# Kernel optimization log

Hardware: AMD Instinct MI355X
Metric: run time of the kernel (lower is better)

The kernel has to match this reference:

```python
import jax, jax.numpy as jnp
import numpy as np

B, FEW, NN = 4096, 5, 64
D = 128            # embed_dim
NSYM = 100000
DM = 2 * D         # d_model = 256
DI = 2 * DM        # support-encoder inner = 512
H = 2 * DM         # LSTMCell hidden = 512
STEPS = 4          # process_steps


def setup_inputs() -> dict:
    key = jax.random.key(0)
    cnt = [0]
    def nk():
        cnt[0] += 1
        return jax.random.fold_in(key, cnt[0])
    def nrm(shape, scale=0.05):
        return jax.random.normal(nk(), shape, dtype=jnp.float32) * scale
    def ridx(shape):
        return jax.random.randint(nk(), shape, 0, NSYM, dtype=jnp.int32)
    inp = {}
    inp['q_l1'] = ridx((B, NN, 2)); inp['q_l2'] = ridx((B, NN, 2))
    inp['q_r1'] = ridx((B, NN, 2)); inp['q_r2'] = ridx((B, NN, 2))
    inp['s_l1'] = ridx((FEW, NN, 2)); inp['s_l2'] = ridx((FEW, NN, 2))
    inp['s_r1'] = ridx((FEW, NN, 2)); inp['s_r2'] = ridx((FEW, NN, 2))
    inp['q_deg_l'] = jax.random.randint(nk(), (B,), 1, NN, dtype=jnp.int32)
    inp['q_deg_r'] = jax.random.randint(nk(), (B,), 1, NN, dtype=jnp.int32)
    inp['s_deg_l'] = jax.random.randint(nk(), (FEW,), 1, NN, dtype=jnp.int32)
    inp['s_deg_r'] = jax.random.randint(nk(), (FEW,), 1, NN, dtype=jnp.int32)
    inp['emb'] = nrm((NSYM + 1, D)).at[NSYM].set(0.0)  # padding_idx row = 0
    inp['gcn_w'] = nrm((D, 2 * D))
    inp['gcn_wb'] = nrm((D,))
    inp['gcn_b'] = jnp.zeros((D,), jnp.float32)
    inp['hop_gate'] = jnp.ones((2,), jnp.float32)
    inp['attn_w'] = nrm((1, D))
    inp['attn_b'] = jnp.zeros((1,), jnp.float32)
    inp['p1_w'] = nrm((DI, DM)); inp['p1_b'] = jnp.zeros((DI,), jnp.float32)
    inp['p2_w'] = nrm((DM, DI)); inp['p2_b'] = jnp.zeros((DM,), jnp.float32)
    inp['ln_g'] = jnp.ones((DM,), jnp.float32); inp['ln_b'] = jnp.zeros((DM,), jnp.float32)
    inp['w_ih'] = nrm((4 * H, DM)); inp['w_hh'] = nrm((4 * H, H))
    inp['b_ih'] = jnp.zeros((4 * H,), jnp.float32); inp['b_hh'] = jnp.zeros((4 * H,), jnp.float32)
    return inp


def _neighbor_encoder(conn, emb, gcn_w, gcn_wb, gcn_b, attn_w, attn_b):
    # conn: [N, NN, 2] (relation id, entity id)
    e = emb[conn]                                     # [N, NN, 2, D]
    concat = e.reshape(conn.shape[0], conn.shape[1], 2 * D)  # cat(rel, ent)
    proj = concat @ gcn_w.T + gcn_wb + gcn_b          # [N, NN, D]
    scores = (proj @ attn_w.T + attn_b)[..., 0]       # [N, NN]
    w = jax.nn.softmax(scores, axis=1)[..., None]
    return jnp.tanh(jnp.sum(proj * w, axis=1))        # [N, D]


def _support_encoder(x, p1_w, p1_b, p2_w, p2_b, ln_g, ln_b):
    out = jax.nn.relu(x @ p1_w.T + p1_b) @ p2_w.T + p2_b
    z = out + x
    mu = jnp.mean(z, axis=-1, keepdims=True)
    var = jnp.var(z, axis=-1, keepdims=True)
    return (z - mu) / jnp.sqrt(var + 1e-6) * ln_g + ln_b


def _query_encoder(support_g, q, w_ih, w_hh, b_ih, b_hh):
    # matching-networks 'process' LSTM attention, STEPS fixed iterations
    h_r = jnp.zeros((q.shape[0], H), q.dtype)
    c = jnp.zeros_like(h_r)
    h = q
    for _ in range(STEPS):
        gates = q @ w_ih.T + b_ih + h_r @ w_hh.T + b_hh
        i, f, g, o = jnp.split(gates, 4, axis=-1)
        c = jax.nn.sigmoid(f) * c + jax.nn.sigmoid(i) * jnp.tanh(g)
        h_cell = jax.nn.sigmoid(o) * jnp.tanh(c)
        h = q + h_cell[:, :DM]
        attn = jax.nn.softmax(h @ support_g.T, axis=1)
        r = attn @ support_g
        h_r = jnp.concatenate([h, r], axis=1)
    return h


def reference(q_l1, q_l2, q_r1, q_r2, s_l1, s_l2, s_r1, s_r2,
              q_deg_l, q_deg_r, s_deg_l, s_deg_r,
              emb, gcn_w, gcn_wb, gcn_b, hop_gate, attn_w, attn_b,
              p1_w, p1_b, p2_w, p2_b, ln_g, ln_b, w_ih, w_hh, b_ih, b_hh):
    ne = lambda conn: _neighbor_encoder(conn, emb, gcn_w, gcn_wb, gcn_b, attn_w, attn_b)
    gw = jax.nn.softmax(hop_gate)
    q_left = gw[0] * ne(q_l1) + gw[1] * ne(q_l2)
    q_right = gw[0] * ne(q_r1) + gw[1] * ne(q_r2)
    s_left = gw[0] * ne(s_l1) + gw[1] * ne(s_l2)
    s_right = gw[0] * ne(s_r1) + gw[1] * ne(s_r2)
    query_neighbor = jnp.concatenate([q_left, q_right], axis=-1)    # [B, DM]
    support_neighbor = jnp.concatenate([s_left, s_right], axis=-1)  # [FEW, DM]
    support_g = _support_encoder(support_neighbor, p1_w, p1_b, p2_w, p2_b, ln_g, ln_b)
    query_g = _query_encoder(support_g, query_neighbor, w_ih, w_hh, b_ih, b_hh)
    support_m = jnp.mean(support_g, axis=0, keepdims=True)          # [1, DM]
    return (query_g @ support_m.T)[:, 0]                            # [B]
```

## Files before the change

### kernel.cpp

```cpp
#include <hip/hip_runtime.h>

typedef unsigned short bf16u;
typedef unsigned char u8;
typedef unsigned int u32;
typedef float f32x4 __attribute__((ext_vector_type(4)));
typedef short bf16x8 __attribute__((ext_vector_type(8)));

__device__ inline float sigmoidf_(float x) { return 1.f / (1.f + __expf(-x)); }
__device__ inline float b2f(bf16u u) { return __uint_as_float(((u32)u) << 16); }
__device__ inline bf16u f2b(float f) {
  u32 i = __float_as_uint(f);
  u32 r = (i + 0x7fffu + ((i >> 16) & 1u)) >> 16;
  return (bf16u)r;
}
__device__ inline u8 enc8(float v) {
  float q = fmaf(v, 512.f, 128.5f);
  q = fminf(fmaxf(q, 0.f), 255.f);
  return (u8)(int)q;
}
__device__ inline float ub0(u32 u) { return (float)(u & 0xffu); }
__device__ inline float ub1(u32 u) { return (float)((u >> 8) & 0xffu); }
__device__ inline float ub2(u32 u) { return (float)((u >> 16) & 0xffu); }
__device__ inline float ub3(u32 u) { return (float)(u >> 24); }

__global__ __launch_bounds__(256) void k_prep(
    const float* __restrict__ gcn_w, const float* __restrict__ attn_w,
    const float* __restrict__ w_ih, const float* __restrict__ w_hh,
    const float* __restrict__ b_ih, const float* __restrict__ b_hh,
    bf16u* __restrict__ Vp, float* __restrict__ uvec,
    bf16u* __restrict__ WWa, bf16u* __restrict__ WWb, float* __restrict__ bsum,
    bf16u* __restrict__ XX)
{
  const int b = blockIdx.x, t = threadIdx.x;
  if (t < 59) XX[(size_t)b * 576 + 517 + t] = 0;
  if (b < 2048) {
    float wi = w_ih[b * 256 + t];
    float wh = w_hh[b * 512 + t];
    WWa[(size_t)b * 576 + t] = f2b(wi);
    WWb[(size_t)b * 576 + t] = f2b(wi + wh);
    WWb[(size_t)b * 576 + 256 + t] = f2b(wh);
    if (t < 59) WWb[(size_t)b * 576 + 517 + t] = 0;
    if (t == 0) bsum[b] = b_ih[b] + b_hh[b];
  } else if (b < 2304) {
    const int o = b - 2048;
    if (t < 128) Vp[o * 128 + t] = f2b(gcn_w[(o & 127) * 256 + ((o >> 7) << 7) + t]);
  } else if (b == 2304) {
    const int col = ((t >> 7) << 7) + (t & 127);
    float acc = 0.f;
    for (int d = 0; d < 128; ++d) acc += gcn_w[d * 256 + col] * attn_w[d];
    uvec[t] = acc;
  }
}

__global__ __launch_bounds__(256) void k_pre_gemm(
    const float* __restrict__ emb, const bf16u* __restrict__ Vp,
    const float* __restrict__ uvec,
    u8* __restrict__ pr, u8* __restrict__ pe,
    float* __restrict__ srel, float* __restrict__ sent)
{
  const int t = threadIdx.x;
  const int row0 = blockIdx.x << 6;
  __shared__ short As[64][136];
  __shared__ union PB {
    short B[128][136];
    u8 ob[64][272];
  } pb;
  __shared__ float us[256];
  us[t] = uvec[t];
  {
    const uint4* src = (const uint4*)Vp;
    #pragma unroll
    for (int s = 0; s < 8; ++s) {
      int f = s * 256 + t;
      *(uint4*)&pb.B[f >> 4][(f & 15) * 8] = src[f];
    }
  }
  #pragma unroll
  for (int s = 0; s < 8; ++s) {
    int f = s * 256 + t;
    int row = f >> 5, q = f & 31;
    int gr = row0 + row; if (gr > 100000) gr = 100000;
    float4 v = *(const float4*)&emb[(size_t)gr * 128 + (q << 2)];
    ushort4 pk;
    pk.x = f2b(v.x); pk.y = f2b(v.y); pk.z = f2b(v.z); pk.w = f2b(v.w);
    *(ushort4*)&As[row][q << 2] = pk;
  }
  __syncthreads();
  {
    const int row = t >> 2, l = t & 3;
    int gr = row0 + row; if (gr > 100000) gr = 100000;
    const short* ar = &As[row][l * 32];
    const float* u0 = &us[l * 32];
    const float* u1 = &us[128 + l * 32];
    float p0 = 0.f, p1 = 0.f;
    #pragma unroll
    for (int i = 0; i < 32; ++i) {
      float e = __uint_as_float(((u32)(unsigned short)ar[i]) << 16);
      p0 += e * u0[i];
      p1 += e * u1[i];
    }
    p0 += __shfl_xor(p0, 1, 64); p0 += __shfl_xor(p0, 2, 64);
    p1 += __shfl_xor(p1, 1, 64); p1 += __shfl_xor(p1, 2, 64);
    if (l == 0) { srel[gr] = p0; sent[gr] = p1; }
  }
  const int wave = t >> 6, lane = t & 63;
  const int quad = lane >> 4, l16 = lane & 15;
  const int wm = (wave >> 1) << 5, wn = (wave & 1) << 6;
  f32x4 acc0[2][4], acc1[2][4];
  #pragma unroll
  for (int i = 0; i < 2; ++i)
    #pragma unroll
    for (int j = 0; j < 4; ++j) {
      acc0[i][j] = (f32x4){0.f, 0.f, 0.f, 0.f};
      acc1[i][j] = (f32x4){0.f, 0.f, 0.f, 0.f};
    }
  #pragma unroll
  for (int kc = 0; kc < 4; ++kc) {
    bf16x8 af[2], bfr[4];
    #pragma unroll
    for (int i = 0; i < 2; ++i)
      af[i] = *(const bf16x8*)&As[wm + i * 16 + l16][kc * 32 + quad * 8];
    #pragma unroll
    for (int j = 0; j < 4; ++j)
      bfr[j] = *(const bf16x8*)&pb.B[wn + j * 16 + l16][kc * 32 + quad * 8];
    #pragma unroll
    for (int i = 0; i < 2; ++i)
      #pragma unroll
      for (int j = 0; j < 4; ++j)
        acc0[i][j] = __builtin_amdgcn_mfma_f32_16x16x32_bf16(af[i], bfr[j], acc0[i][j], 0, 0, 0);
  }
  __syncthreads();
  {
    const uint4* src = (const uint4*)(Vp + 128 * 128);
    #pragma unroll
    for (int s = 0; s < 8; ++s) {
      int f = s * 256 + t;
      *(uint4*)&pb.B[f >> 4][(f & 15) * 8] = src[f];
    }
  }
  __syncthreads();
  #pragma unroll
  for (int kc = 0; kc < 4; ++kc) {
    bf16x8 af[2], bfr[4];
    #pragma unroll
    for (int i = 0; i < 2; ++i)
      af[i] = *(const bf16x8*)&As[wm + i * 16 + l16][kc * 32 + quad * 8];
    #pragma unroll
    for (int j = 0; j < 4; ++j)
      bfr[j] = *(const bf16x8*)&pb.B[wn + j * 16 + l16][kc * 32 + quad * 8];
    #pragma unroll
    for (int i = 0; i < 2; ++i)
      #pragma unroll
      for (int j = 0; j < 4; ++j)
        acc1[i][j] = __builtin_amdgcn_mfma_f32_16x16x32_bf16(af[i], bfr[j], acc1[i][j], 0, 0, 0);
  }
  __syncthreads();
  #pragma unroll
  for (int j = 0; j < 4; ++j) {
    const int col = wn + j * 16 + l16;
    #pragma unroll
    for (int i = 0; i < 2; ++i) {
      #pragma unroll
      for (int r = 0; r < 4; ++r) {
        int row = wm + i * 16 + quad * 4 + r;
        pb.ob[row][col] = enc8(acc0[i][j][r]);
        pb.ob[row][128 + col] = enc8(acc1[i][j][r]);
      }
    }
  }
  __syncthreads();
  #pragma unroll
  for (int s = 0; s < 4; ++s) {
    int c = s * 256 + t;
    int row = c >> 4, part = c & 15;
    int gr = row0 + row;
    if (gr <= 100000) {
      uint4 v = *(const uint4*)&pb.ob[row][part * 16];
      if (part < 8) *(uint4*)&pr[(size_t)gr * 128 + part * 16] = v;
      else          *(uint4*)&pe[(size_t)gr * 128 + (part - 8) * 16] = v;
    }
  }
}

__global__ __launch_bounds__(256) void k_neighbor(
    const int* __restrict__ q_l1, const int* __restrict__ q_l2,
    const int* __restrict__ q_r1, const int* __restrict__ q_r2,
    const int* __restrict__ s_l1, const int* __restrict__ s_l2,
    const int* __restrict__ s_r1, const int* __restrict__ s_r2,
    const u8* __restrict__ pr, const u8* __restrict__ pe,
    const float* __restrict__ srel, const float* __restrict__ sent,
    const float* __restrict__ gcn_wb, const float* __restrict__ gcn_b,
    const float* __restrict__ hop_gate,
    float* __restrict__ qn, float* __restrict__ sn, bf16u* __restrict__ XX)
{
  const int b = blockIdx.x, t = threadIdx.x;
  const int *cA, *cB; float* outp; bf16u* xxp; int n, coloff;
  if (b < 4096)      { cA = q_l1; cB = q_l2; n = b;        outp = qn; xxp = XX; coloff = 0; }
  else if (b < 8192) { cA = q_r1; cB = q_r2; n = b - 4096; outp = qn; xxp = XX; coloff = 128; }
  else if (b < 8197) { cA = s_l1; cB = s_l2; n = b - 8192; outp = sn; xxp = 0;  coloff = 0; }
  else               { cA = s_r1; cB = s_r2; n = b - 8197; outp = sn; xxp = 0;  coloff = 128; }
  __shared__ int idxA[64][2], idxB[64][2];
  __shared__ float wA[64], wB[64];
  __shared__ float red[2][8][16][8];
  if (t < 128) {
    const int hop = t >> 6, nn = t & 63;
    const int* conn = hop ? cB : cA;
    int rel = conn[(n * 64 + nn) * 2 + 0];
    int ent = conn[(n * 64 + nn) * 2 + 1];
    int (*idx)[2] = hop ? idxB : idxA;
    idx[nn][0] = rel; idx[nn][1] = ent;
    float sc = srel[rel] + sent[ent];
    float m = sc;
    #pragma unroll
    for (int off = 32; off; off >>= 1) m = fmaxf(m, __shfl_xor(m, off, 64));
    float e = __expf(sc - m);
    float s = e;
    #pragma unroll
    for (int off = 32; off; off >>= 1) s += __shfl_xor(s, off, 64);
    (hop ? wB : wA)[nn] = e / s;
  }
  __syncthreads();
  {
    const int hop = t >> 7, g = (t >> 4) & 7, p = t & 15;
    const int (*idx)[2] = hop ? idxB : idxA;
    const float* w = hop ? wB : wA;
    uint2 ra[8], rb[8];
    #pragma unroll
    for (int kk = 0; kk < 8; ++kk) {
      int k = g + (kk << 3);
      ra[kk] = *(const uint2*)&pr[(size_t)idx[k][0] * 128 + p * 8];
      rb[kk] = *(const uint2*)&pe[(size_t)idx[k][1] * 128 + p * 8];
    }
    float a[8];
    #pragma unroll
    for (int c = 0; c < 8; ++c) a[c] = 0.f;
    #pragma unroll
    for (int kk = 0; kk < 8; ++kk) {
      float wk = w[g + (kk << 3)];
      a[0] += wk * (ub0(ra[kk].x) + ub0(rb[kk].x));
      a[1] += wk * (ub1(ra[kk].x) + ub1(rb[kk].x));
      a[2] += wk * (ub2(ra[kk].x) + ub2(rb[kk].x));
      a[3] += wk * (ub3(ra[kk].x) + ub3(rb[kk].x));
      a[4] += wk * (ub0(ra[kk].y) + ub0(rb[kk].y));
      a[5] += wk * (ub1(ra[kk].y) + ub1(rb[kk].y));
      a[6] += wk * (ub2(ra[kk].y) + ub2(rb[kk].y));
      a[7] += wk * (ub3(ra[kk].y) + ub3(rb[kk].y));
    }
    *(float4*)&red[hop][g][p][0] = (float4){a[0], a[1], a[2], a[3]};
    *(float4*)&red[hop][g][p][4] = (float4){a[4], a[5], a[6], a[7]};
  }
  __syncthreads();
  if (t < 128) {
    const int d = t, p = d >> 3, cq = d & 7;
    float sA = 0.f, sB = 0.f;
    #pragma unroll
    for (int g = 0; g < 8; ++g) {
      sA += red[0][g][p][cq];
      sB += red[1][g][p][cq];
    }
    float accA = sA * (1.f / 512.f) - 0.5f;
    float accB = sB * (1.f / 512.f) - 0.5f;
    float bias = gcn_wb[d] + gcn_b[d];
    float g0 = hop_gate[0], g1 = hop_gate[1];
    float mx = fmaxf(g0, g1);
    float e0 = __expf(g0 - mx), e1 = __expf(g1 - mx);
    float inv = 1.f / (e0 + e1);
    float v = e0 * inv * tanhf(bias + accA) + e1 * inv * tanhf(bias + accB);
    outp[n * 256 + coloff + d] = v;
    if (xxp) xxp[(size_t)n * 576 + coloff + d] = f2b(v);
  }
}

__global__ __launch_bounds__(256) void k_sup1(
    const float* __restrict__ sn, const float* __restrict__ p1_w,
    const float* __restrict__ p1_b, float* __restrict__ h1)
{
  const int r = blockIdx.x >> 3, j0 = (blockIdx.x & 7) << 6;
  const int t = threadIdx.x;
  __shared__ float xs[256];
  xs[t] = sn[r * 256 + t];
  __syncthreads();
  const int j = j0 + (t >> 2), q = t & 3;
  const float* wr = p1_w + (size_t)j * 256 + q * 64;
  float acc = 0.f;
  #pragma unroll
  for (int k = 0; k < 64; ++k) acc += xs[q * 64 + k] * wr[k];
  acc += __shfl_xor(acc, 1, 64);
  acc += __shfl_xor(acc, 2, 64);
  if (q == 0) h1[r * 512 + j] = fmaxf(acc + p1_b[j], 0.f);
}

__global__ __launch_bounds__(256) void k_sup2(
    const float* __restrict__ sn, const float* __restrict__ h1,
    const float* __restrict__ p2_w, const float* __restrict__ p2_b,
    const float* __restrict__ ln_g, const float* __restrict__ ln_b,
    float* __restrict__ sg)
{
  const int r = blockIdx.x, t = threadIdx.x;
  const int lane = t & 63, wave = t >> 6;
  __shared__ float hs[512];
  __shared__ float zs[256];
  __shared__ float r1[4], r2[4];
  hs[t] = h1[r * 512 + t];
  hs[t + 256] = h1[r * 512 + 256 + t];
  __syncthreads();
  const int q = t & 3;
  #pragma unroll
  for (int jc = 0; jc < 4; ++jc) {
    int j = jc * 64 + (t >> 2);
    const float* wr = p2_w + (size_t)j * 512 + q * 128;
    float acc = 0.f;
    #pragma unroll
    for (int k = 0; k < 128; ++k) acc += hs[q * 128 + k] * wr[k];
    acc += __shfl_xor(acc, 1, 64);
    acc += __shfl_xor(acc, 2, 64);
    if (q == 0) zs[j] = acc + p2_b[j] + sn[r * 256 + j];
  }
  __syncthreads();
  float v = zs[t];
  float s1 = v, s2 = v * v;
  #pragma unroll
  for (int off = 32; off; off >>= 1) { s1 += __shfl_xor(s1, off, 64); s2 += __shfl_xor(s2, off, 64); }
  if (lane == 0) { r1[wave] = s1; r2[wave] = s2; }
  __syncthreads();
  float S1 = r1[0] + r1[1] + r1[2] + r1[3];
  float S2 = r2[0] + r2[1] + r2[2] + r2[3];
  float mu = S1 * (1.f / 256.f);
  float var = S2 * (1.f / 256.f) - mu * mu;
  sg[r * 256 + t] = (v - mu) * rsqrtf(var + 1e-6f) * ln_g[t] + ln_b[t];
}

__global__ __launch_bounds__(256) void k_sg2(
    const float* __restrict__ sg, const float* __restrict__ w_hh,
    bf16u* __restrict__ WWb, float* __restrict__ sm)
{
  __shared__ float s[5][256];
  const int t = threadIdx.x;
  for (int i = t; i < 1280; i += 256) s[i >> 8][i & 255] = sg[i];
  __syncthreads();
  if (blockIdx.x == 0)
    sm[t] = (s[0][t] + s[1][t] + s[2][t] + s[3][t] + s[4][t]) * 0.2f;
  const int j = (blockIdx.x << 6) + (t >> 2), q = t & 3;
  const float4* wr = (const float4*)(w_hh + (size_t)j * 512 + 256 + q * 64);
  float a[5] = {0.f, 0.f, 0.f, 0.f, 0.f};
  #pragma unroll
  for (int kk = 0; kk < 16; ++kk) {
    float4 w = wr[kk];
    int k = q * 64 + kk * 4;
    #pragma unroll
    for (int r = 0; r < 5; ++r)
      a[r] += s[r][k] * w.x + s[r][k+1] * w.y + s[r][k+2] * w.z + s[r][k+3] * w.w;
  }
  #pragma unroll
  for (int r = 0; r < 5; ++r) {
    a[r] += __shfl_xor(a[r], 1, 64);
    a[r] += __shfl_xor(a[r], 2, 64);
  }
  if (q == 0) {
    #pragma unroll
    for (int r = 0; r < 5; ++r)
      WWb[(size_t)j * 576 + 512 + r] = f2b(a[r]);
  }
}

__global__ __launch_bounds__(256) void k_gates_mfma(
    const bf16u* __restrict__ XX, const bf16u* __restrict__ WW,
    const float* __restrict__ bsum, bf16u* __restrict__ gates, int kchunks)
{
  const int t = threadIdx.x;
  const int wave = t >> 6, lane = t & 63;
  const int quad = lane >> 4, l16 = lane & 15;
  const int wm = (wave >> 1) << 6, wn = (wave & 1) << 6;
  const int lin = (blockIdx.x & 7) * 64 + (blockIdx.x >> 3);
  const int row0 = (lin >> 4) << 7;
  const int col0 = (lin & 15) << 7;
  __shared__ short As[128][40];
  __shared__ short Bs[128][40];
  f32x4 acc[4][4];
  #pragma unroll
  for (int i = 0; i < 4; ++i)
    #pragma unroll
    for (int j = 0; j < 4; ++j) acc[i][j] = (f32x4){0.f, 0.f, 0.f, 0.f};

  const int srow = t >> 1, shalf = t & 1;
  const bf16u* xp = XX + (size_t)(row0 + srow) * 576 + shalf * 16;
  const bf16u* wp = WW + (size_t)(col0 + srow) * 576 + shalf * 16;

  uint4 x0 = *(const uint4*)(xp);
  uint4 x1 = *(const uint4*)(xp + 8);
  uint4 w0 = *(const uint4*)(wp);
  uint4 w1 = *(const uint4*)(wp + 8);

  for (int kc = 0; kc < kchunks; ++kc) {
    __syncthreads();
    *(uint4*)&As[srow][shalf * 16] = x0;
    *(uint4*)&As[srow][shalf * 16 + 8] = x1;
    *(uint4*)&Bs[srow][shalf * 16] = w0;
    *(uint4*)&Bs[srow][shalf * 16 + 8] = w1;
    __syncthreads();
    if (kc + 1 < kchunks) {
      x0 = *(const uint4*)(xp + (kc+1) * 32);
      x1 = *(const uint4*)(xp + (kc+1) * 32 + 8);
      w0 = *(const uint4*)(wp + (kc+1) * 32);
      w1 = *(const uint4*)(wp + (kc+1) * 32 + 8);
    }
    bf16x8 af[4], bfr[4];
    #pragma unroll
    for (int i = 0; i < 4; ++i)
      af[i] = *(const bf16x8*)&As[wm + i * 16 + l16][quad * 8];
    #pragma unroll
    for (int j = 0; j < 4; ++j)
      bfr[j] = *(const bf16x8*)&Bs[wn + j * 16 + l16][quad * 8];
    #pragma unroll
    for (int i = 0; i < 4; ++i)
      #pragma unroll
      for (int j = 0; j < 4; ++j)
        acc[i][j] = __builtin_amdgcn_mfma_f32_16x16x32_bf16(af[i], bfr[j], acc[i][j], 0, 0, 0);
  }

  #pragma unroll
  for (int j = 0; j < 4; ++j) {
    const int col = col0 + wn + j * 16 + l16;
    const float bs = bsum[col];
    #pragma unroll
    for (int i = 0; i < 4; ++i) {
      #pragma unroll
      for (int r = 0; r < 4; ++r) {
        int row = row0 + wm + i * 16 + quad * 4 + r;
        gates[(size_t)row * 2048 + col] = f2b(acc[i][j][r] + bs);
      }
    }
  }
}

__global__ __launch_bounds__(256) void k_cell(
    const bf16u* __restrict__ gates, const float* __restrict__ qn,
    float* __restrict__ c, bf16u* __restrict__ XX,
    const float* __restrict__ sg, const float* __restrict__ sm,
    float* __restrict__ out, int step)
{
  __shared__ float red[4][6];
  const int b = blockIdx.x, t = threadIdx.x;
  const int lane = t & 63, wave = t >> 6;
  const bf16u* g = gates + (size_t)b * 2048;
  float i0 = b2f(g[t]),       f0 = b2f(g[512 + t]), gg0 = b2f(g[1024 + t]), o0 = b2f(g[1536 + t]);
  float i1 = b2f(g[256 + t]), f1 = b2f(g[768 + t]), gg1 = b2f(g[1280 + t]);
  float co0 = step ? c[b * 512 + t] : 0.f;
  float co1 = step ? c[b * 512 + 256 + t] : 0.f;
  float c0 = sigmoidf_(f0) * co0 + sigmoidf_(i0) * tanhf(gg0);
  float c1 = sigmoidf_(f1) * co1 + sigmoidf_(i1) * tanhf(gg1);
  c[b * 512 + t] = c0;
  c[b * 512 + 256 + t] = c1;
  float hcv = sigmoidf_(o0) * tanhf(c0);
  float h = qn[b * 256 + t] + hcv;
  if (step < 3) {
    XX[(size_t)b * 576 + 256 + t] = f2b(hcv);
    float dots[5];
    #pragma unroll
    for (int s = 0; s < 5; ++s) dots[s] = h * sg[s * 256 + t];
    #pragma unroll
    for (int off = 32; off; off >>= 1) {
      #pragma unroll
      for (int s = 0; s < 5; ++s) dots[s] += __shfl_xor(dots[s], off, 64);
    }
    if (lane == 0) {
      #pragma unroll
      for (int s = 0; s < 5; ++s) red[wave][s] = dots[s];
    }
    __syncthreads();
    #pragma unroll
    for (int s = 0; s < 5; ++s)
      dots[s] = red[0][s] + red[1][s] + red[2][s] + red[3][s];
    float m = dots[0];
    #pragma unroll
    for (int s = 1; s < 5; ++s) m = fmaxf(m, dots[s]);
    float sum = 0.f;
    #pragma unroll
    for (int s = 0; s < 5; ++s) sum += __expf(dots[s] - m);
    if (t < 5) {
      float dv = (t == 1) ? dots[1] : (t == 2) ? dots[2] : (t == 3) ? dots[3]
               : (t == 4) ? dots[4] : dots[0];
      XX[(size_t)b * 576 + 512 + t] = f2b(__expf(dv - m) / sum);
    }
  } else {
    float v = h * sm[t];
    #pragma unroll
    for (int off = 32; off; off >>= 1) v += __shfl_xor(v, off, 64);
    if (lane == 0) red[wave][0] = v;
    __syncthreads();
    if (t == 0) out[b] = red[0][0] + red[1][0] + red[2][0] + red[3][0];
  }
}

extern "C" void kernel_launch(void* const* d_in, const int* in_sizes, int n_in,
                              void* d_out, int out_size, void* d_ws, size_t ws_size,
                              hipStream_t stream)
{
  (void)in_sizes; (void)n_in; (void)out_size; (void)ws_size;
  const int *q_l1 = (const int*)d_in[0], *q_l2 = (const int*)d_in[1];
  const int *q_r1 = (const int*)d_in[2], *q_r2 = (const int*)d_in[3];
  const int *s_l1 = (const int*)d_in[4], *s_l2 = (const int*)d_in[5];
  const int *s_r1 = (const int*)d_in[6], *s_r2 = (const int*)d_in[7];
  const float* emb      = (const float*)d_in[12];
  const float* gcn_w    = (const float*)d_in[13];
  const float* gcn_wb   = (const float*)d_in[14];
  const float* gcn_b    = (const float*)d_in[15];
  const float* hop_gate = (const float*)d_in[16];
  const float* attn_w   = (const float*)d_in[17];
  const float* p1_w = (const float*)d_in[19];
  const float* p1_b = (const float*)d_in[20];
  const float* p2_w = (const float*)d_in[21];
  const float* p2_b = (const float*)d_in[22];
  const float* ln_g = (const float*)d_in[23];
  const float* ln_b = (const float*)d_in[24];
  const float* w_ih = (const float*)d_in[25];
  const float* w_hh = (const float*)d_in[26];
  const float* b_ih = (const float*)d_in[27];
  const float* b_hh = (const float*)d_in[28];

  char* base = (char*)d_ws;
  size_t off = 0;
  auto alloc = [&](size_t bytes) -> char* {
    char* r = base + off;
    off = (off + bytes + 255) & ~(size_t)255;
    return r;
  };
  u8* pr       = (u8*)alloc(100001ull * 128);
  u8* pe       = (u8*)alloc(100001ull * 128);
  float* srel  = (float*)alloc(100001ull * 4);
  float* sent  = (float*)alloc(100001ull * 4);
  float* uvec  = (float*)alloc(256 * 4);
  bf16u* Vp    = (bf16u*)alloc(256 * 128 * 2);
  float* qn    = (float*)alloc(4096ull * 256 * 4);
  float* sn    = (float*)alloc(5 * 256 * 4);
  float* sg    = (float*)alloc(5 * 256 * 4);
  float* sm    = (float*)alloc(256 * 4);
  float* h1b   = (float*)alloc(5 * 512 * 4);
  bf16u* XX    = (bf16u*)alloc(4096ull * 576 * 2);
  bf16u* WWa   = (bf16u*)alloc(2048ull * 576 * 2);
  bf16u* WWb   = (bf16u*)alloc(2048ull * 576 * 2);
  float* bsum  = (float*)alloc(2048 * 4);
  bf16u* gates = (bf16u*)alloc(4096ull * 2048 * 2);
  float* cbuf  = (float*)alloc(4096ull * 512 * 4);

  k_prep<<<4096, 256, 0, stream>>>(gcn_w, attn_w, w_ih, w_hh, b_ih, b_hh,
                                   Vp, uvec, WWa, WWb, bsum, XX);
  k_pre_gemm<<<1563, 256, 0, stream>>>(emb, Vp, uvec, pr, pe, srel, sent);
  k_neighbor<<<8202, 256, 0, stream>>>(q_l1, q_l2, q_r1, q_r2, s_l1, s_l2, s_r1, s_r2,
                                       pr, pe, srel, sent, gcn_wb, gcn_b, hop_gate,
                                       qn, sn, XX);
  k_sup1<<<40, 256, 0, stream>>>(sn, p1_w, p1_b, h1b);
  k_sup2<<<5, 256, 0, stream>>>(sn, h1b, p2_w, p2_b, ln_g, ln_b, sg);
  k_sg2<<<32, 256, 0, stream>>>(sg, w_hh, WWb, sm);

  for (int step = 0; step < 4; ++step) {
    if (step == 0)
      k_gates_mfma<<<512, 256, 0, stream>>>(XX, WWa, bsum, gates, 8);
    else
      k_gates_mfma<<<512, 256, 0, stream>>>(XX, WWb, bsum, gates, 17);
    k_cell<<<4096, 256, 0, stream>>>(gates, qn, cbuf, XX, sg, sm, (float*)d_out, step);
  }
}
```

Before: 338.6 us.

## Precompute loop-invariant query gate contribution once and shrink per-step GEMM K

The query-neighbor part of the LSTM input, multiplied by (W_ih+W_hh) plus bias, is the same at every step. It is now computed once into a G1 buffer alongside the step-0 gates GEMM. Steps 1-3 then run a GEMM over K=320 (hidden state plus attention weights) and add G1 back, where before each step ran K=544 over the concatenated XX. This removes redundant MFMA work and operand reads per step, at the cost of a 16 MB bf16 G1 buffer read in each step's epilogue and an extra rounding to bf16.

```diff
diff --git a/kernel.cpp b/kernel.cpp
--- a/kernel.cpp
+++ b/kernel.cpp
@@ -28,18 +28,18 @@
     const float* __restrict__ w_ih, const float* __restrict__ w_hh,
     const float* __restrict__ b_ih, const float* __restrict__ b_hh,
     bf16u* __restrict__ Vp, float* __restrict__ uvec,
-    bf16u* __restrict__ WWa, bf16u* __restrict__ WWb, float* __restrict__ bsum,
-    bf16u* __restrict__ XX)
+    bf16u* __restrict__ WWa, bf16u* __restrict__ WWc, bf16u* __restrict__ WW2,
+    float* __restrict__ bsum, bf16u* __restrict__ XX2)
 {
   const int b = blockIdx.x, t = threadIdx.x;
-  if (t < 59) XX[(size_t)b * 576 + 517 + t] = 0;
+  if (t < 59) XX2[(size_t)b * 320 + 261 + t] = 0;
   if (b < 2048) {
     float wi = w_ih[b * 256 + t];
     float wh = w_hh[b * 512 + t];
-    WWa[(size_t)b * 576 + t] = f2b(wi);
-    WWb[(size_t)b * 576 + t] = f2b(wi + wh);
-    WWb[(size_t)b * 576 + 256 + t] = f2b(wh);
-    if (t < 59) WWb[(size_t)b * 576 + 517 + t] = 0;
+    WWa[(size_t)b * 256 + t] = f2b(wi);
+    WWc[(size_t)b * 256 + t] = f2b(wi + wh);
+    WW2[(size_t)b * 320 + t] = f2b(wh);
+    if (t < 59) WW2[(size_t)b * 320 + 261 + t] = 0;
     if (t == 0) bsum[b] = b_ih[b] + b_hh[b];
   } else if (b < 2304) {
     const int o = b - 2048;
@@ -267,7 +267,7 @@
     float inv = 1.f / (e0 + e1);
     float v = e0 * inv * tanhf(bias + accA) + e1 * inv * tanhf(bias + accB);
     outp[n * 256 + coloff + d] = v;
-    if (xxp) xxp[(size_t)n * 576 + coloff + d] = f2b(v);
+    if (xxp) xxp[(size_t)n * 256 + coloff + d] = f2b(v);
   }
 }
 
@@ -332,7 +332,7 @@
 
 __global__ __launch_bounds__(256) void k_sg2(
     const float* __restrict__ sg, const float* __restrict__ w_hh,
-    bf16u* __restrict__ WWb, float* __restrict__ sm)
+    bf16u* __restrict__ WW2, float* __restrict__ sm)
 {
   __shared__ float s[5][256];
   const int t = threadIdx.x;
@@ -359,19 +359,20 @@
   if (q == 0) {
     #pragma unroll
     for (int r = 0; r < 5; ++r)
-      WWb[(size_t)j * 576 + 512 + r] = f2b(a[r]);
-  }
-}
-
-__global__ __launch_bounds__(256) void k_gates_mfma(
-    const bf16u* __restrict__ XX, const bf16u* __restrict__ WW,
-    const float* __restrict__ bsum, bf16u* __restrict__ gates, int kchunks)
+      WW2[(size_t)j * 320 + 256 + r] = f2b(a[r]);
+  }
+}
+
+template <int XSTRIDE>
+__device__ inline void gates_body(
+    const bf16u* __restrict__ X, const bf16u* __restrict__ W,
+    const float* __restrict__ bsum, const bf16u* __restrict__ add,
+    bf16u* __restrict__ out, int kchunks, int lin)
 {
   const int t = threadIdx.x;
   const int wave = t >> 6, lane = t & 63;
   const int quad = lane >> 4, l16 = lane & 15;
   const int wm = (wave >> 1) << 6, wn = (wave & 1) << 6;
-  const int lin = (blockIdx.x & 7) * 64 + (blockIdx.x >> 3);
   const int row0 = (lin >> 4) << 7;
   const int col0 = (lin & 15) << 7;
   __shared__ short As[128][40];
@@ -383,8 +384,8 @@
     for (int j = 0; j < 4; ++j) acc[i][j] = (f32x4){0.f, 0.f, 0.f, 0.f};
 
   const int srow = t >> 1, shalf = t & 1;
-  const bf16u* xp = XX + (size_t)(row0 + srow) * 576 + shalf * 16;
-  const bf16u* wp = WW + (size_t)(col0 + srow) * 576 + shalf * 16;
+  const bf16u* xp = X + (size_t)(row0 + srow) * XSTRIDE + shalf * 16;
+  const bf16u* wp = W + (size_t)(col0 + srow) * XSTRIDE + shalf * 16;
 
   uint4 x0 = *(const uint4*)(xp);
   uint4 x1 = *(const uint4*)(xp + 8);
@@ -421,21 +422,44 @@
   #pragma unroll
   for (int j = 0; j < 4; ++j) {
     const int col = col0 + wn + j * 16 + l16;
-    const float bs = bsum[col];
+    const float bs = add ? 0.f : bsum[col];
     #pragma unroll
     for (int i = 0; i < 4; ++i) {
       #pragma unroll
       for (int r = 0; r < 4; ++r) {
         int row = row0 + wm + i * 16 + quad * 4 + r;
-        gates[(size_t)row * 2048 + col] = f2b(acc[i][j][r] + bs);
+        float base = add ? b2f(add[(size_t)row * 2048 + col]) : bs;
+        out[(size_t)row * 2048 + col] = f2b(acc[i][j][r] + base);
       }
     }
   }
+}
+
+__global__ __launch_bounds__(256) void k_gates0(
+    const bf16u* __restrict__ XX, const bf16u* __restrict__ WWa,
+    const bf16u* __restrict__ WWc, const float* __restrict__ bsum,
+    bf16u* __restrict__ gates, bf16u* __restrict__ G1)
+{
+  const int b = blockIdx.x;
+  const int base = b & 511;
+  const int lin = (base & 7) * 64 + (base >> 3);
+  if (b < 512)
+    gates_body<256>(XX, WWa, bsum, (const bf16u*)nullptr, gates, 8, lin);
+  else
+    gates_body<256>(XX, WWc, bsum, (const bf16u*)nullptr, G1, 8, lin);
+}
+
+__global__ __launch_bounds__(256) void k_gates_step(
+    const bf16u* __restrict__ XX2, const bf16u* __restrict__ WW2,
+    const bf16u* __restrict__ G1, bf16u* __restrict__ gates)
+{
+  const int lin = (blockIdx.x & 7) * 64 + (blockIdx.x >> 3);
+  gates_body<320>(XX2, WW2, (const float*)nullptr, G1, gates, 10, lin);
 }
 
 __global__ __launch_bounds__(256) void k_cell(
     const bf16u* __restrict__ gates, const float* __restrict__ qn,
-    float* __restrict__ c, bf16u* __restrict__ XX,
+    float* __restrict__ c, bf16u* __restrict__ XX2,
     const float* __restrict__ sg, const float* __restrict__ sm,
     float* __restrict__ out, int step)
 {
@@ -454,7 +478,7 @@
   float hcv = sigmoidf_(o0) * tanhf(c0);
   float h = qn[b * 256 + t] + hcv;
   if (step < 3) {
-    XX[(size_t)b * 576 + 256 + t] = f2b(hcv);
+    XX2[(size_t)b * 320 + t] = f2b(hcv);
     float dots[5];
     #pragma unroll
     for (int s = 0; s < 5; ++s) dots[s] = h * sg[s * 256 + t];
@@ -480,7 +504,7 @@
     if (t < 5) {
       float dv = (t == 1) ? dots[1] : (t == 2) ? dots[2] : (t == 3) ? dots[3]
                : (t == 4) ? dots[4] : dots[0];
-      XX[(size_t)b * 576 + 512 + t] = f2b(__expf(dv - m) / sum);
+      XX2[(size_t)b * 320 + 256 + t] = f2b(__expf(dv - m) / sum);
     }
   } else {
     float v = h * sm[t];
@@ -536,28 +560,30 @@
   float* sg    = (float*)alloc(5 * 256 * 4);
   float* sm    = (float*)alloc(256 * 4);
   float* h1b   = (float*)alloc(5 * 512 * 4);
-  bf16u* XX    = (bf16u*)alloc(4096ull * 576 * 2);
-  bf16u* WWa   = (bf16u*)alloc(2048ull * 576 * 2);
-  bf16u* WWb   = (bf16u*)alloc(2048ull * 576 * 2);
+  bf16u* XX    = (bf16u*)alloc(4096ull * 256 * 2);
+  bf16u* XX2   = (bf16u*)alloc(4096ull * 320 * 2);
+  bf16u* WWa   = (bf16u*)alloc(2048ull * 256 * 2);
+  bf16u* WWc   = (bf16u*)alloc(2048ull * 256 * 2);
+  bf16u* WW2   = (bf16u*)alloc(2048ull * 320 * 2);
   float* bsum  = (float*)alloc(2048 * 4);
   bf16u* gates = (bf16u*)alloc(4096ull * 2048 * 2);
+  bf16u* G1    = (bf16u*)alloc(4096ull * 2048 * 2);
   float* cbuf  = (float*)alloc(4096ull * 512 * 4);
 
   k_prep<<<4096, 256, 0, stream>>>(gcn_w, attn_w, w_ih, w_hh, b_ih, b_hh,
-                                   Vp, uvec, WWa, WWb, bsum, XX);
+                                   Vp, uvec, WWa, WWc, WW2, bsum, XX2);
   k_pre_gemm<<<1563, 256, 0, stream>>>(emb, Vp, uvec, pr, pe, srel, sent);
   k_neighbor<<<8202, 256, 0, stream>>>(q_l1, q_l2, q_r1, q_r2, s_l1, s_l2, s_r1, s_r2,
                                        pr, pe, srel, sent, gcn_wb, gcn_b, hop_gate,
                                        qn, sn, XX);
   k_sup1<<<40, 256, 0, stream>>>(sn, p1_w, p1_b, h1b);
   k_sup2<<<5, 256, 0, stream>>>(sn, h1b, p2_w, p2_b, ln_g, ln_b, sg);
-  k_sg2<<<32, 256, 0, stream>>>(sg, w_hh, WWb, sm);
-
-  for (int step = 0; step < 4; ++step) {
-    if (step == 0)
-      k_gates_mfma<<<512, 256, 0, stream>>>(XX, WWa, bsum, gates, 8);
-    else
-      k_gates_mfma<<<512, 256, 0, stream>>>(XX, WWb, bsum, gates, 17);
-    k_cell<<<4096, 256, 0, stream>>>(gates, qn, cbuf, XX, sg, sm, (float*)d_out, step);
-  }
-}
+  k_sg2<<<32, 256, 0, stream>>>(sg, w_hh, WW2, sm);
+
+  k_gates0<<<1024, 256, 0, stream>>>(XX, WWa, WWc, bsum, gates, G1);
+  k_cell<<<4096, 256, 0, stream>>>(gates, qn, cbuf, XX2, sg, sm, (float*)d_out, 0);
+  for (int step = 1; step < 4; ++step) {
+    k_gates_step<<<512, 256, 0, stream>>>(XX2, WW2, G1, gates);
+    k_cell<<<4096, 256, 0, stream>>>(gates, qn, cbuf, XX2, sg, sm, (float*)d_out, step);
+  }
+}
```

After: 363.1 us. 7.2% more time.
